# Kernel tuning notes

Hardware: AMD Instinct MI355X
Metric: run time of the kernel (lower is better)

Reference implementation:

```python
import jax, jax.numpy as jnp
import numpy as np

N_SPECIES = 4  # species ids 0..3


def setup_inputs() -> dict:
    key = jax.random.key(0)
    k1, k2, k3, k4 = jax.random.split(key, 4)
    NTA, O, NMAX = 65536, 512, 512
    rho = jax.random.normal(k1, (NTA, O), dtype=jnp.float32)
    # per-species expert Linear(O -> NMAX): weights stacked [S, O, NMAX], bias [S, NMAX]
    W = jax.random.normal(k2, (N_SPECIES, O, NMAX), dtype=jnp.float32) * (1.0 / np.sqrt(O))
    b = jax.random.normal(k3, (N_SPECIES, NMAX), dtype=jnp.float32) * 0.01
    symbols = jax.random.randint(k4, (NTA,), 0, N_SPECIES, dtype=jnp.int32)
    return {"rho": rho, "W": W, "b": b, "symbols": symbols}


def reference(rho, W, b, symbols):
    # Faithful to Gj.forward: coeff[mask] = expert_spe(rho[mask]) for each species.
    # Vectorized form: apply each species' Linear to all atoms (dense GEMM),
    # then select per-atom by species mask. Loop is over the small fixed
    # species set (4), not over data dims.
    NTA = rho.shape[0]
    nmax = W.shape[-1]
    coeff = jnp.zeros((NTA, nmax), dtype=rho.dtype)
    for spe in range(W.shape[0]):
        y = rho @ W[spe] + b[spe]            # [NTA, nmax]
        mask = (symbols == spe)[:, None]      # [NTA, 1]
        coeff = jnp.where(mask, y, coeff)
    return coeff
```

## Files before the change

### kernel.cpp

```cpp
#include <hip/hip_runtime.h>


#define NTA   65536
#define DIM_O 512
#define NMAXD 512
#define NSPE  4
#define BM    64
#define BK    64

typedef __attribute__((ext_vector_type(4))) float  f32x4;
typedef __attribute__((ext_vector_type(8))) short  bf16x8;
typedef __attribute__((ext_vector_type(4))) short  bf16x4;

__device__ __forceinline__ short f2bf(float f) {
    unsigned u = __builtin_bit_cast(unsigned, f);
    u += 0x7FFFu + ((u >> 16) & 1u);
    return (short)(u >> 16);
}

__global__ void build_lists_kernel(const int* __restrict__ sym,
                                   int* __restrict__ counts,
                                   int* __restrict__ lists) {
    int i = blockIdx.x * 256 + threadIdx.x;
    int s = sym[i];
    int lane = threadIdx.x & 63;
    #pragma unroll
    for (int spe = 0; spe < NSPE; ++spe) {
        unsigned long long m = __ballot(s == spe);
        if (m == 0ull) continue;
        int leader = __ffsll(m) - 1;
        int base = 0;
        if (lane == leader) base = atomicAdd(&counts[spe], __popcll(m));
        base = __shfl(base, leader);
        if (s == spe) {
            int pos = __popcll(m & ((1ull << lane) - 1ull));
            lists[spe * NTA + base + pos] = i;
        }
    }
}

__global__ void pack_w_kernel(const float* __restrict__ W, short* __restrict__ Wp,
                              int* __restrict__ counts) {
    if (blockIdx.x == 0 && threadIdx.x < NSPE) counts[threadIdx.x] = 0;
    int idx = blockIdx.x * 256 + threadIdx.x;
    int j  = idx & 7;
    int l  = (idx >> 3) & 63;
    int nb = (idx >> 9) & 31;
    int kb = (idx >> 14) & 15;
    int s  = idx >> 18;
    int k = kb * 32 + (l >> 4) * 8 + j;
    int n = nb * 16 + (l & 15);
    Wp[idx] = f2bf(W[((size_t)s * DIM_O + k) * NMAXD + n]);
}

__global__ __launch_bounds__(512, 4)
void gemm_kernel(const float* __restrict__ rho,
                 const short* __restrict__ Wp,
                 const float* __restrict__ bias,
                 const int*  __restrict__ counts,
                 const int*  __restrict__ lists,
                 float* __restrict__ out)
{
    const int s   = blockIdx.x & 3;
    const int mb  = blockIdx.x >> 2;
    const int cnt = counts[s];
    const int row0 = mb * BM;
    if (row0 >= cnt) return;
    int rows_here = cnt - row0; if (rows_here > BM) rows_here = BM;

    __shared__ int aidx[BM];
    __shared__ __align__(16) short Abuf[64 * 64 * 8];

    const int tid  = threadIdx.x;
    const int lane = tid & 63;
    const int w    = tid >> 6;
    const int lrow = lane & 15;
    const int lgr  = lane >> 4;

    if (tid < BM)
        aidx[tid] = lists[s * NTA + row0 + ((tid < rows_here) ? tid : 0)];
    __syncthreads();

    {
        const int srow  = tid >> 3;
        const int scol8 = tid & 7;
        const float* gsrc = rho + (size_t)aidx[srow] * DIM_O + scol8 * 4;
        const int c0   = scol8 >> 1;
        const int roww = srow ^ ((c0 & 3) << 1);
        const int dof  = (scol8 & 1) * 4;

        f32x4 v[16];
        #pragma unroll
        for (int r = 0; r < 16; ++r)
            v[r] = *(const f32x4*)(gsrc + r * 32);
        #pragma unroll
        for (int r = 0; r < 16; ++r) {
            bf16x4 a;
            #pragma unroll
            for (int q = 0; q < 4; ++q) a[q] = f2bf(v[r][q]);
            *(bf16x4*)&Abuf[((r * 4 + c0) * 64 + roww) * 8 + dof] = a;
        }
    }
    __syncthreads();

    const short* wbase = Wp + ((size_t)s * 512 + w * 4) * 512 + lane * 8;

    f32x4 acc[4][4];
    #pragma unroll
    for (int m = 0; m < 4; ++m)
        #pragma unroll
        for (int n = 0; n < 4; ++n) acc[m][n] = (f32x4)0.0f;

    #pragma unroll
    for (int kt = 0; kt < 8; ++kt) {
        bf16x8 bfr[2][4];
        #pragma unroll
        for (int ks = 0; ks < 2; ++ks)
            #pragma unroll
            for (int nf = 0; nf < 4; ++nf)
                bfr[ks][nf] = *(const bf16x8*)
                    (wbase + (size_t)((kt * 2 + ks) * 32 + nf) * 512);
        #pragma unroll
        for (int ks = 0; ks < 2; ++ks) {
            #pragma unroll
            for (int mf = 0; mf < 4; ++mf) {
                const int c = kt * 8 + ks * 4 + lgr;
                const int r = (mf * 16 + lrow) ^ ((lgr & 3) << 1);
                const bf16x8 afrag = *(const bf16x8*)&Abuf[(c * 64 + r) * 8];
                #pragma unroll
                for (int nf = 0; nf < 4; ++nf)
                    acc[mf][nf] = __builtin_amdgcn_mfma_f32_16x16x32_bf16(
                        afrag, bfr[ks][nf], acc[mf][nf], 0, 0, 0);
            }
        }
    }

    float bv[4];
    #pragma unroll
    for (int nf = 0; nf < 4; ++nf)
        bv[nf] = bias[s * NMAXD + w * 64 + nf * 16 + lrow];
    #pragma unroll
    for (int mf = 0; mf < 4; ++mf) {
        #pragma unroll
        for (int q = 0; q < 4; ++q) {
            const int r = mf * 16 + lgr * 4 + q;
            if (r < rows_here) {
                float* orow = out + (size_t)aidx[r] * NMAXD + w * 64 + lrow;
                #pragma unroll
                for (int nf = 0; nf < 4; ++nf)
                    orow[nf * 16] = acc[mf][nf][q] + bv[nf];
            }
        }
    }
}

extern "C" void kernel_launch(void* const* d_in, const int* in_sizes, int n_in,
                              void* d_out, int out_size, void* d_ws, size_t ws_size,
                              hipStream_t stream) {
    const float* rho = (const float*)d_in[0];
    const float* W   = (const float*)d_in[1];
    const float* b   = (const float*)d_in[2];
    const int*   sym = (const int*)d_in[3];
    float* out = (float*)d_out;

    int*   counts = (int*)d_ws;
    int*   lists  = (int*)((char*)d_ws + 1024);
    short* Wp     = (short*)((char*)d_ws + 1024 + (size_t)NSPE * NTA * 4);

    pack_w_kernel<<<(NSPE * DIM_O * NMAXD) / 256, 256, 0, stream>>>(W, Wp, counts);
    build_lists_kernel<<<NTA / 256, 256, 0, stream>>>(sym, counts, lists);
    gemm_kernel<<<NSPE * (NTA / BM), 512, 0, stream>>>(rho, Wp, b, counts, lists, out);
}
```

Baseline: 126.8 us.

## Make GEMM persistent with double-buffered A tiles and register prefetch

```diff
diff --git a/kernel.cpp b/kernel.cpp
--- a/kernel.cpp
+++ b/kernel.cpp
@@ -5,8 +5,6 @@
 #define DIM_O 512
 #define NMAXD 512
 #define NSPE  4
-#define BM    64
-#define BK    64
 
 typedef __attribute__((ext_vector_type(4))) float  f32x4;
 typedef __attribute__((ext_vector_type(8))) short  bf16x8;
@@ -53,7 +51,7 @@
     Wp[idx] = f2bf(W[((size_t)s * DIM_O + k) * NMAXD + n]);
 }
 
-__global__ __launch_bounds__(512, 4)
+__global__ __launch_bounds__(1024, 4)
 void gemm_kernel(const float* __restrict__ rho,
                  const short* __restrict__ Wp,
                  const float* __restrict__ bias,
@@ -61,15 +59,15 @@
                  const int*  __restrict__ lists,
                  float* __restrict__ out)
 {
-    const int s   = blockIdx.x & 3;
-    const int mb  = blockIdx.x >> 2;
+    const int s = blockIdx.x & 3;
+    const int g = blockIdx.x >> 2;
     const int cnt = counts[s];
-    const int row0 = mb * BM;
-    if (row0 >= cnt) return;
-    int rows_here = cnt - row0; if (rows_here > BM) rows_here = BM;
+    const int ntiles = (cnt + 63) >> 6;
+    if (g >= ntiles) return;
+    const int ntb = min(8, (ntiles - g + 63) >> 6);
 
-    __shared__ int aidx[BM];
-    __shared__ __align__(16) short Abuf[64 * 64 * 8];
+    __shared__ int aidxm[512];
+    __shared__ __align__(16) short Abuf[2][64 * 64 * 8];
 
     const int tid  = threadIdx.x;
     const int lane = tid & 63;
@@ -77,79 +75,93 @@
     const int lrow = lane & 15;
     const int lgr  = lane >> 4;
 
-    if (tid < BM)
-        aidx[tid] = lists[s * NTA + row0 + ((tid < rows_here) ? tid : 0)];
+    if (tid < ntb * 64) {
+        const int t = tid >> 6, r = tid & 63;
+        const int idx = (g + t * 64) * 64 + r;
+        aidxm[tid] = lists[s * NTA + min(idx, cnt - 1)];
+    }
     __syncthreads();
 
+    const int srow   = tid >> 4;
+    const int scol16 = tid & 15;
+    const int c0     = scol16 >> 1;
+    const int h      = scol16 & 1;
+    const int roww   = srow ^ ((c0 & 3) << 1);
+
+    const short* wbase = Wp + ((size_t)s * 512 + w * 2) * 512 + lane * 8;
+    const float bv0 = bias[s * NMAXD + w * 32 + lrow];
+    const float bv1 = bias[s * NMAXD + w * 32 + 16 + lrow];
+
+    f32x4 st[8];
+
     {
-        const int srow  = tid >> 3;
-        const int scol8 = tid & 7;
-        const float* gsrc = rho + (size_t)aidx[srow] * DIM_O + scol8 * 4;
-        const int c0   = scol8 >> 1;
-        const int roww = srow ^ ((c0 & 3) << 1);
-        const int dof  = (scol8 & 1) * 4;
-
-        f32x4 v[16];
+        const float* gsrc = rho + (size_t)aidxm[srow] * DIM_O + scol16 * 4;
         #pragma unroll
-        for (int r = 0; r < 16; ++r)
-            v[r] = *(const f32x4*)(gsrc + r * 32);
+        for (int r = 0; r < 8; ++r) st[r] = *(const f32x4*)(gsrc + r * 64);
         #pragma unroll
-        for (int r = 0; r < 16; ++r) {
+        for (int r = 0; r < 8; ++r) {
             bf16x4 a;
             #pragma unroll
-            for (int q = 0; q < 4; ++q) a[q] = f2bf(v[r][q]);
-            *(bf16x4*)&Abuf[((r * 4 + c0) * 64 + roww) * 8 + dof] = a;
+            for (int q = 0; q < 4; ++q) a[q] = f2bf(st[r][q]);
+            *(bf16x4*)&Abuf[0][((r * 8 + c0) * 64 + roww) * 8 + h * 4] = a;
         }
     }
     __syncthreads();
 
-    const short* wbase = Wp + ((size_t)s * 512 + w * 4) * 512 + lane * 8;
+    for (int t = 0; t < ntb; ++t) {
+        const int buf = t & 1;
+        const bool hn = (t + 1 < ntb);
 
-    f32x4 acc[4][4];
-    #pragma unroll
-    for (int m = 0; m < 4; ++m)
+        if (hn) {
+            const float* gsrc =
+                rho + (size_t)aidxm[(t + 1) * 64 + srow] * DIM_O + scol16 * 4;
+            #pragma unroll
+            for (int r = 0; r < 8; ++r) st[r] = *(const f32x4*)(gsrc + r * 64);
+        }
+
+        f32x4 acc[4][2];
         #pragma unroll
-        for (int n = 0; n < 4; ++n) acc[m][n] = (f32x4)0.0f;
+        for (int m = 0; m < 4; ++m) { acc[m][0] = (f32x4)0.0f; acc[m][1] = (f32x4)0.0f; }
 
-    #pragma unroll
-    for (int kt = 0; kt < 8; ++kt) {
-        bf16x8 bfr[2][4];
         #pragma unroll
-        for (int ks = 0; ks < 2; ++ks)
-            #pragma unroll
-            for (int nf = 0; nf < 4; ++nf)
-                bfr[ks][nf] = *(const bf16x8*)
-                    (wbase + (size_t)((kt * 2 + ks) * 32 + nf) * 512);
-        #pragma unroll
-        for (int ks = 0; ks < 2; ++ks) {
+        for (int kb = 0; kb < 16; ++kb) {
+            const bf16x8 bf0 = *(const bf16x8*)(wbase + (size_t)(kb * 32    ) * 512);
+            const bf16x8 bf1 = *(const bf16x8*)(wbase + (size_t)(kb * 32 + 1) * 512);
             #pragma unroll
             for (int mf = 0; mf < 4; ++mf) {
-                const int c = kt * 8 + ks * 4 + lgr;
-                const int r = (mf * 16 + lrow) ^ ((lgr & 3) << 1);
-                const bf16x8 afrag = *(const bf16x8*)&Abuf[(c * 64 + r) * 8];
-                #pragma unroll
-                for (int nf = 0; nf < 4; ++nf)
-                    acc[mf][nf] = __builtin_amdgcn_mfma_f32_16x16x32_bf16(
-                        afrag, bfr[ks][nf], acc[mf][nf], 0, 0, 0);
+                const int c = kb * 4 + lgr;
+                const int r = (mf * 16 + lrow) ^ (lgr << 1);
+                const bf16x8 afrag = *(const bf16x8*)&Abuf[buf][(c * 64 + r) * 8];
+                acc[mf][0] = __builtin_amdgcn_mfma_f32_16x16x32_bf16(
+                    afrag, bf0, acc[mf][0], 0, 0, 0);
+                acc[mf][1] = __builtin_amdgcn_mfma_f32_16x16x32_bf16(
+                    afrag, bf1, acc[mf][1], 0, 0, 0);
             }
         }
-    }
 
-    float bv[4];
-    #pragma unroll
-    for (int nf = 0; nf < 4; ++nf)
-        bv[nf] = bias[s * NMAXD + w * 64 + nf * 16 + lrow];
-    #pragma unroll
-    for (int mf = 0; mf < 4; ++mf) {
+        const int rbase = (g + t * 64) * 64;
         #pragma unroll
-        for (int q = 0; q < 4; ++q) {
-            const int r = mf * 16 + lgr * 4 + q;
-            if (r < rows_here) {
-                float* orow = out + (size_t)aidx[r] * NMAXD + w * 64 + lrow;
+        for (int mf = 0; mf < 4; ++mf) {
+            #pragma unroll
+            for (int q = 0; q < 4; ++q) {
+                const int r = mf * 16 + lgr * 4 + q;
+                if (rbase + r < cnt) {
+                    float* orow = out + (size_t)aidxm[t * 64 + r] * NMAXD + w * 32 + lrow;
+                    orow[0]  = acc[mf][0][q] + bv0;
+                    orow[16] = acc[mf][1][q] + bv1;
+                }
+            }
+        }
+
+        if (hn) {
+            #pragma unroll
+            for (int r = 0; r < 8; ++r) {
+                bf16x4 a;
                 #pragma unroll
-                for (int nf = 0; nf < 4; ++nf)
-                    orow[nf * 16] = acc[mf][nf][q] + bv[nf];
+                for (int q = 0; q < 4; ++q) a[q] = f2bf(st[r][q]);
+                *(bf16x4*)&Abuf[buf ^ 1][((r * 8 + c0) * 64 + roww) * 8 + h * 4] = a;
             }
+            __syncthreads();
         }
     }
 }
@@ -169,5 +181,5 @@
 
     pack_w_kernel<<<(NSPE * DIM_O * NMAXD) / 256, 256, 0, stream>>>(W, Wp, counts);
     build_lists_kernel<<<NTA / 256, 256, 0, stream>>>(sym, counts, lists);
-    gemm_kernel<<<NSPE * (NTA / BM), 512, 0, stream>>>(rho, Wp, b, counts, lists, out);
+    gemm_kernel<<<NSPE * 64, 1024, 0, stream>>>(rho, Wp, b, counts, lists, out);
 }
```

Result: slower. 302.0 us (+138.1%).

## Make GEMM persistent over packed species tiles with register-prefetched gathers

Applied to the files above, without the earlier changes.

```diff
diff --git a/kernel.cpp b/kernel.cpp
--- a/kernel.cpp
+++ b/kernel.cpp
@@ -5,8 +5,6 @@
 #define DIM_O 512
 #define NMAXD 512
 #define NSPE  4
-#define BM    64
-#define BK    64
 
 typedef __attribute__((ext_vector_type(4))) float  f32x4;
 typedef __attribute__((ext_vector_type(8))) short  bf16x8;
@@ -16,6 +14,12 @@
     unsigned u = __builtin_bit_cast(unsigned, f);
     u += 0x7FFFu + ((u >> 16) & 1u);
     return (short)(u >> 16);
+}
+
+__device__ __forceinline__ void bar_lds() {
+    asm volatile("s_waitcnt lgkmcnt(0)" ::: "memory");
+    __builtin_amdgcn_s_barrier();
+    __builtin_amdgcn_sched_barrier(0);
 }
 
 __global__ void build_lists_kernel(const int* __restrict__ sym,
@@ -53,7 +57,7 @@
     Wp[idx] = f2bf(W[((size_t)s * DIM_O + k) * NMAXD + n]);
 }
 
-__global__ __launch_bounds__(512, 4)
+__global__ __launch_bounds__(512, 2)
 void gemm_kernel(const float* __restrict__ rho,
                  const short* __restrict__ Wp,
                  const float* __restrict__ bias,
@@ -61,97 +65,126 @@
                  const int*  __restrict__ lists,
                  float* __restrict__ out)
 {
-    const int s   = blockIdx.x & 3;
-    const int mb  = blockIdx.x >> 2;
-    const int cnt = counts[s];
-    const int row0 = mb * BM;
-    if (row0 >= cnt) return;
-    int rows_here = cnt - row0; if (rows_here > BM) rows_here = BM;
-
-    __shared__ int aidx[BM];
-    __shared__ __align__(16) short Abuf[64 * 64 * 8];
-
-    const int tid  = threadIdx.x;
+    const int b   = blockIdx.x;
+    const int tid = threadIdx.x;
     const int lane = tid & 63;
     const int w    = tid >> 6;
     const int lrow = lane & 15;
     const int lgr  = lane >> 4;
 
-    if (tid < BM)
-        aidx[tid] = lists[s * NTA + row0 + ((tid < rows_here) ? tid : 0)];
+    const int c0x = counts[0], c1x = counts[1], c2x = counts[2], c3x = counts[3];
+    const int P1 = (c0x + 63) >> 6;
+    const int P2 = P1 + ((c1x + 63) >> 6);
+    const int P3 = P2 + ((c2x + 63) >> 6);
+    const int ntot = P3 + ((c3x + 63) >> 6);
+
+    __shared__ int aidxA[2][64];
+    __shared__ __align__(16) short Abuf[64 * 64 * 8];
+
+    const int srow  = tid >> 3;
+    const int scol8 = tid & 7;
+    const int cc0   = scol8 >> 1;
+    const int roww  = srow ^ ((cc0 & 3) << 1);
+    const int dof   = (scol8 & 1) * 4;
+
+    #define TILE_INFO(ti, s_, mb_, cnt_)                                   \
+        {   s_ = ((ti) >= P1) + ((ti) >= P2) + ((ti) >= P3);               \
+            mb_ = (ti) - (s_ == 0 ? 0 : s_ == 1 ? P1 : s_ == 2 ? P2 : P3); \
+            cnt_ = (s_ == 0 ? c0x : s_ == 1 ? c1x : s_ == 2 ? c2x : c3x); }
+
+    f32x4 st[16];
+
+    {
+        int s, mb, cnt; TILE_INFO(b, s, mb, cnt);
+        if (tid < 64) aidxA[0][tid] = lists[s * NTA + min(mb * 64 + tid, cnt - 1)];
+    }
     __syncthreads();
-
     {
-        const int srow  = tid >> 3;
-        const int scol8 = tid & 7;
-        const float* gsrc = rho + (size_t)aidx[srow] * DIM_O + scol8 * 4;
-        const int c0   = scol8 >> 1;
-        const int roww = srow ^ ((c0 & 3) << 1);
-        const int dof  = (scol8 & 1) * 4;
-
-        f32x4 v[16];
-        #pragma unroll
-        for (int r = 0; r < 16; ++r)
-            v[r] = *(const f32x4*)(gsrc + r * 32);
+        const float* g = rho + (size_t)aidxA[0][srow] * DIM_O + scol8 * 4;
+        #pragma unroll
+        for (int r = 0; r < 16; ++r) st[r] = *(const f32x4*)(g + r * 32);
+    }
+
+    int p = 0;
+    for (int ti = b; ti < ntot; ti += 256, p ^= 1) {
+        int s, mb, cnt; TILE_INFO(ti, s, mb, cnt);
+        const int rows_here = min(64, cnt - mb * 64);
+
+        bar_lds();
+
         #pragma unroll
         for (int r = 0; r < 16; ++r) {
             bf16x4 a;
             #pragma unroll
-            for (int q = 0; q < 4; ++q) a[q] = f2bf(v[r][q]);
-            *(bf16x4*)&Abuf[((r * 4 + c0) * 64 + roww) * 8 + dof] = a;
-        }
-    }
-    __syncthreads();
-
-    const short* wbase = Wp + ((size_t)s * 512 + w * 4) * 512 + lane * 8;
-
-    f32x4 acc[4][4];
-    #pragma unroll
-    for (int m = 0; m < 4; ++m)
-        #pragma unroll
-        for (int n = 0; n < 4; ++n) acc[m][n] = (f32x4)0.0f;
-
-    #pragma unroll
-    for (int kt = 0; kt < 8; ++kt) {
-        bf16x8 bfr[2][4];
-        #pragma unroll
-        for (int ks = 0; ks < 2; ++ks)
-            #pragma unroll
-            for (int nf = 0; nf < 4; ++nf)
-                bfr[ks][nf] = *(const bf16x8*)
-                    (wbase + (size_t)((kt * 2 + ks) * 32 + nf) * 512);
-        #pragma unroll
-        for (int ks = 0; ks < 2; ++ks) {
-            #pragma unroll
-            for (int mf = 0; mf < 4; ++mf) {
-                const int c = kt * 8 + ks * 4 + lgr;
-                const int r = (mf * 16 + lrow) ^ ((lgr & 3) << 1);
-                const bf16x8 afrag = *(const bf16x8*)&Abuf[(c * 64 + r) * 8];
+            for (int q = 0; q < 4; ++q) a[q] = f2bf(st[r][q]);
+            *(bf16x4*)&Abuf[((r * 4 + cc0) * 64 + roww) * 8 + dof] = a;
+        }
+
+        const int tn = ti + 256;
+        if (tn < ntot) {
+            int s2, mb2, cnt2; TILE_INFO(tn, s2, mb2, cnt2);
+            if (tid < 64)
+                aidxA[p ^ 1][tid] = lists[s2 * NTA + min(mb2 * 64 + tid, cnt2 - 1)];
+        }
+        bar_lds();
+
+        if (tn < ntot) {
+            const float* g = rho + (size_t)aidxA[p ^ 1][srow] * DIM_O + scol8 * 4;
+            #pragma unroll
+            for (int r = 0; r < 16; ++r) st[r] = *(const f32x4*)(g + r * 32);
+        }
+
+        const short* wbase = Wp + ((size_t)s * 512 + w * 4) * 512 + lane * 8;
+
+        f32x4 acc[4][4];
+        #pragma unroll
+        for (int m = 0; m < 4; ++m)
+            #pragma unroll
+            for (int n = 0; n < 4; ++n) acc[m][n] = (f32x4)0.0f;
+
+        #pragma unroll
+        for (int kt = 0; kt < 8; ++kt) {
+            bf16x8 bfr[2][4];
+            #pragma unroll
+            for (int ks = 0; ks < 2; ++ks)
                 #pragma unroll
                 for (int nf = 0; nf < 4; ++nf)
-                    acc[mf][nf] = __builtin_amdgcn_mfma_f32_16x16x32_bf16(
-                        afrag, bfr[ks][nf], acc[mf][nf], 0, 0, 0);
+                    bfr[ks][nf] = *(const bf16x8*)
+                        (wbase + (size_t)((kt * 2 + ks) * 32 + nf) * 512);
+            #pragma unroll
+            for (int ks = 0; ks < 2; ++ks) {
+                #pragma unroll
+                for (int mf = 0; mf < 4; ++mf) {
+                    const int c = kt * 8 + ks * 4 + lgr;
+                    const int r = (mf * 16 + lrow) ^ ((lgr & 3) << 1);
+                    const bf16x8 afrag = *(const bf16x8*)&Abuf[(c * 64 + r) * 8];
+                    #pragma unroll
+                    for (int nf = 0; nf < 4; ++nf)
+                        acc[mf][nf] = __builtin_amdgcn_mfma_f32_16x16x32_bf16(
+                            afrag, bfr[ks][nf], acc[mf][nf], 0, 0, 0);
+                }
             }
         }
-    }
-
-    float bv[4];
-    #pragma unroll
-    for (int nf = 0; nf < 4; ++nf)
-        bv[nf] = bias[s * NMAXD + w * 64 + nf * 16 + lrow];
-    #pragma unroll
-    for (int mf = 0; mf < 4; ++mf) {
-        #pragma unroll
-        for (int q = 0; q < 4; ++q) {
-            const int r = mf * 16 + lgr * 4 + q;
-            if (r < rows_here) {
-                float* orow = out + (size_t)aidx[r] * NMAXD + w * 64 + lrow;
-                #pragma unroll
-                for (int nf = 0; nf < 4; ++nf)
-                    orow[nf * 16] = acc[mf][nf][q] + bv[nf];
+
+        float bv[4];
+        #pragma unroll
+        for (int nf = 0; nf < 4; ++nf)
+            bv[nf] = bias[s * NMAXD + w * 64 + nf * 16 + lrow];
+        #pragma unroll
+        for (int mf = 0; mf < 4; ++mf) {
+            #pragma unroll
+            for (int q = 0; q < 4; ++q) {
+                const int r = mf * 16 + lgr * 4 + q;
+                if (r < rows_here) {
+                    float* orow = out + (size_t)aidxA[p][r] * NMAXD + w * 64 + lrow;
+                    #pragma unroll
+                    for (int nf = 0; nf < 4; ++nf)
+                        orow[nf * 16] = acc[mf][nf][q] + bv[nf];
+                }
             }
         }
     }
+    #undef TILE_INFO
 }
 
 extern "C" void kernel_launch(void* const* d_in, const int* in_sizes, int n_in,
@@ -169,5 +202,5 @@
 
     pack_w_kernel<<<(NSPE * DIM_O * NMAXD) / 256, 256, 0, stream>>>(W, Wp, counts);
     build_lists_kernel<<<NTA / 256, 256, 0, stream>>>(sym, counts, lists);
-    gemm_kernel<<<NSPE * (NTA / BM), 512, 0, stream>>>(rho, Wp, b, counts, lists, out);
-}
+    gemm_kernel<<<256, 512, 0, stream>>>(rho, Wp, b, counts, lists, out);
+}
```

Result: slower. 134.4 us (+6.0%).
